# Kernel tuning notes

Measured on AMD Instinct MI355X. Metric: run time of the kernel, lower is better.

The kernel has to match this reference:

```python
import jax, jax.numpy as jnp
import numpy as np

N_NODES = 50000
N_EDGES = 800000
IN_CH = 128
HID = 128
NUM_GRAPHS = 512
BN_EPS = 1e-5


def setup_inputs() -> dict:
    key = jax.random.key(0)
    ks = jax.random.split(key, 16)
    x = jax.random.normal(ks[0], (N_NODES, IN_CH), dtype=jnp.float32)
    edge_index = jax.random.randint(ks[1], (2, N_EDGES), 0, N_NODES, dtype=jnp.int64)
    batch = jnp.sort(jax.random.randint(ks[2], (N_NODES,), 0, NUM_GRAPHS, dtype=jnp.int64))

    def glorot(k, shape):
        fan_in = shape[1]
        return jax.random.normal(k, shape, dtype=jnp.float32) / jnp.sqrt(jnp.float32(fan_in))

    # SAGEConv1: lin_l (aggr path, with bias), lin_r (root path, no bias)
    W1l = glorot(ks[3], (HID, IN_CH)); b1 = jnp.zeros((HID,), jnp.float32)
    W1r = glorot(ks[4], (HID, IN_CH))
    # SAGEConv2
    W2l = glorot(ks[5], (HID, HID)); b2 = jnp.zeros((HID,), jnp.float32)
    W2r = glorot(ks[6], (HID, HID))
    # MLP tail
    lin1_w = glorot(ks[7], (HID, HID)); lin1_b = jnp.zeros((HID,), jnp.float32)
    lin2_w = glorot(ks[8], (2, HID)); lin2_b = jnp.zeros((2,), jnp.float32)
    # BatchNorm1d (eval mode, running stats)
    gamma = jnp.ones((HID,), jnp.float32)
    beta = jnp.zeros((HID,), jnp.float32)
    running_mean = jax.random.normal(ks[9], (HID,), dtype=jnp.float32) * 0.1
    running_var = jax.random.uniform(ks[10], (HID,), dtype=jnp.float32, minval=0.5, maxval=1.5)
    return {
        "x": x, "edge_index": edge_index, "batch": batch,
        "W1l": W1l, "b1": b1, "W1r": W1r,
        "W2l": W2l, "b2": b2, "W2r": W2r,
        "lin1_w": lin1_w, "lin1_b": lin1_b,
        "lin2_w": lin2_w, "lin2_b": lin2_b,
        "gamma": gamma, "beta": beta,
        "running_mean": running_mean, "running_var": running_var,
    }


def _sage_conv(x, src, dst, Wl, bl, Wr):
    # mean-aggregate neighbor features (message flows src -> dst)
    n = x.shape[0]
    agg = jax.ops.segment_sum(x[src], dst, num_segments=n)  # [N, d]
    cnt = jax.ops.segment_sum(jnp.ones((src.shape[0], 1), x.dtype), dst, num_segments=n)
    mean = agg / jnp.maximum(cnt, 1.0)
    return mean @ Wl.T + bl + x @ Wr.T


def reference(x, edge_index, batch, W1l, b1, W1r, W2l, b2, W2r,
              lin1_w, lin1_b, lin2_w, lin2_b, gamma, beta,
              running_mean, running_var):
    src, dst = edge_index[0], edge_index[1]
    h = _sage_conv(x, src, dst, W1l, b1, W1r)      # [N, HID]
    h = _sage_conv(h, src, dst, W2l, b2, W2r)      # [N, HID]
    h = jax.ops.segment_sum(h, batch, num_segments=NUM_GRAPHS)  # global_add_pool -> [G, HID]
    h = h @ lin1_w.T + lin1_b
    # BatchNorm1d in eval mode (running stats)
    h = (h - running_mean) * jax.lax.rsqrt(running_var + BN_EPS) * gamma + beta
    h = jax.nn.relu(h)
    h = h @ lin2_w.T + lin2_b                      # [G, 2]
    # Dropout is identity in eval mode
    return h
```

## Files before the change

### kernel.cpp

```cpp
#include <hip/hip_runtime.h>
#include <hip/hip_bf16.h>

#define NN 50000
#define NE 800000
#define HID 128
#define NG 512
#define BN_EPS 1e-5f

typedef __attribute__((ext_vector_type(8))) short bf16x8;
typedef __attribute__((ext_vector_type(4))) float f32x4;

__device__ __forceinline__ ushort f2bf(float f) {
    uint u = __float_as_uint(f);
    uint r = (u + 0x7fffu + ((u >> 16) & 1u)) >> 16;
    return (ushort)r;
}
__device__ __forceinline__ float bf_lo(uint v) { return __uint_as_float(v << 16); }
__device__ __forceinline__ float bf_hi(uint v) { return __uint_as_float(v & 0xffff0000u); }

__global__ __launch_bounds__(256) void hist_kernel(const int* __restrict__ ei,
                                                   int E, int* __restrict__ deg,
                                                   int* __restrict__ rank) {
    int e = blockIdx.x * 256 + threadIdx.x;
    if (e >= E) return;
    int dst = ei[E + e];
    rank[e] = atomicAdd(&deg[dst], 1);
}

__global__ __launch_bounds__(256) void scan1_kernel(const int* __restrict__ deg,
                                                    int* __restrict__ row_start,
                                                    int* __restrict__ bsums, int n) {
    __shared__ int s[256];
    int i = blockIdx.x * 256 + threadIdx.x;
    int v = (i < n) ? deg[i] : 0;
    s[threadIdx.x] = v;
    __syncthreads();
    for (int off = 1; off < 256; off <<= 1) {
        int t = (threadIdx.x >= off) ? s[threadIdx.x - off] : 0;
        __syncthreads();
        s[threadIdx.x] += t;
        __syncthreads();
    }
    if (i < n) row_start[i] = s[threadIdx.x] - v;
    if (threadIdx.x == 255) bsums[blockIdx.x] = s[255];
}

__global__ __launch_bounds__(256) void scan2_kernel(int* __restrict__ bsums, int nb) {
    __shared__ int s[256];
    int v = (threadIdx.x < nb) ? bsums[threadIdx.x] : 0;
    s[threadIdx.x] = v;
    __syncthreads();
    for (int off = 1; off < 256; off <<= 1) {
        int t = (threadIdx.x >= off) ? s[threadIdx.x - off] : 0;
        __syncthreads();
        s[threadIdx.x] += t;
        __syncthreads();
    }
    if (threadIdx.x < nb) bsums[threadIdx.x] = s[threadIdx.x] - v;
}

__global__ __launch_bounds__(256) void scan3_kernel(int* __restrict__ row_start,
                                                    const int* __restrict__ bsums, int n) {
    int i = blockIdx.x * 256 + threadIdx.x;
    if (i < n) row_start[i] += bsums[blockIdx.x];
}

__global__ __launch_bounds__(256) void fill_kernel(const int* __restrict__ ei, int E,
                                                   const int* __restrict__ row_start,
                                                   const int* __restrict__ rank,
                                                   int* __restrict__ srclist) {
    int e = blockIdx.x * 256 + threadIdx.x;
    if (e >= E) return;
    int src = ei[e];
    int dst = ei[E + e];
    srclist[row_start[dst] + rank[e]] = src;
}

__global__ __launch_bounds__(256) void convert_bf16_kernel(const float* __restrict__ in,
                                                           ushort* __restrict__ out, int n4) {
    int i = blockIdx.x * 256 + threadIdx.x;
    if (i >= n4) return;
    float4 v = ((const float4*)in)[i];
    ushort4 o;
    o.x = f2bf(v.x);
    o.y = f2bf(v.y);
    o.z = f2bf(v.z);
    o.w = f2bf(v.w);
    ((ushort4*)out)[i] = o;
}

__global__ __launch_bounds__(64) void wprep_kernel(const float* __restrict__ W0,
                                                   const float* __restrict__ W1,
                                                   const float* __restrict__ W2,
                                                   const float* __restrict__ W3,
                                                   ushort* __restrict__ Wp) {
    int b = blockIdx.x;
    int m = b >> 5;
    int g = b & 31;
    int tile = g >> 2;
    int chunk = g & 3;
    int lane = threadIdx.x;
    const float* W = (m == 0) ? W0 : (m == 1) ? W1 : (m == 2) ? W2 : W3;
    int col = tile * 16 + (lane & 15);
    int k0 = chunk * 32 + (lane >> 4) * 8;
    ushort* dst = Wp + ((size_t)b * 64 + lane) * 8;
#pragma unroll
    for (int j = 0; j < 8; ++j) dst[j] = f2bf(W[col * HID + k0 + j]);
}

__global__ __launch_bounds__(256) void aggregate_kernel(const ushort* __restrict__ feat,
                                                        const int* __restrict__ row_start,
                                                        const int* __restrict__ deg,
                                                        const int* __restrict__ srclist,
                                                        ushort* __restrict__ mean, int n) {
    int node = blockIdx.x * 4 + (threadIdx.x >> 6);
    if (node >= n) return;
    int lane = threadIdx.x & 63;
    int cl = lane & 15;
    int sub = lane >> 4;
    const uint4* fb = (const uint4*)feat;
    int s0 = row_start[node];
    int d = deg[node];

    float a[8];
#pragma unroll
    for (int i = 0; i < 8; ++i) a[i] = 0.f;

    int j = 0;
    for (; j + 8 <= d; j += 8) {
        int i0 = srclist[s0 + j + sub];
        int i1 = srclist[s0 + j + 4 + sub];
        uint4 v0 = fb[(size_t)i0 * 16 + cl];
        uint4 v1 = fb[(size_t)i1 * 16 + cl];
        a[0] += bf_lo(v0.x) + bf_lo(v1.x);
        a[1] += bf_hi(v0.x) + bf_hi(v1.x);
        a[2] += bf_lo(v0.y) + bf_lo(v1.y);
        a[3] += bf_hi(v0.y) + bf_hi(v1.y);
        a[4] += bf_lo(v0.z) + bf_lo(v1.z);
        a[5] += bf_hi(v0.z) + bf_hi(v1.z);
        a[6] += bf_lo(v0.w) + bf_lo(v1.w);
        a[7] += bf_hi(v0.w) + bf_hi(v1.w);
    }
    for (; j < d; j += 4) {
        int idx = j + sub;
        bool valid = idx < d;
        int safe = valid ? idx : (d - 1);
        int src = srclist[s0 + safe];
        uint4 v = fb[(size_t)src * 16 + cl];
        float s = valid ? 1.f : 0.f;
        a[0] += s * bf_lo(v.x);
        a[1] += s * bf_hi(v.x);
        a[2] += s * bf_lo(v.y);
        a[3] += s * bf_hi(v.y);
        a[4] += s * bf_lo(v.z);
        a[5] += s * bf_hi(v.z);
        a[6] += s * bf_lo(v.w);
        a[7] += s * bf_hi(v.w);
    }

#pragma unroll
    for (int i = 0; i < 8; ++i) {
        float v = a[i];
        v += __shfl_xor(v, 16);
        v += __shfl_xor(v, 32);
        a[i] = v;
    }

    if (sub == 0) {
        float inv = 1.0f / fmaxf((float)d, 1.0f);
        uint4 o;
        o.x = (uint)f2bf(a[0] * inv) | ((uint)f2bf(a[1] * inv) << 16);
        o.y = (uint)f2bf(a[2] * inv) | ((uint)f2bf(a[3] * inv) << 16);
        o.z = (uint)f2bf(a[4] * inv) | ((uint)f2bf(a[5] * inv) << 16);
        o.w = (uint)f2bf(a[6] * inv) | ((uint)f2bf(a[7] * inv) << 16);
        ((uint4*)mean)[(size_t)node * 16 + cl] = o;
    }
}

template <bool POOL>
__global__ __launch_bounds__(256) void sage_gemm_mfma(const ushort* __restrict__ Amean,
                                                      const ushort* __restrict__ Aroot,
                                                      const ushort* __restrict__ WpL,
                                                      const float* __restrict__ bias,
                                                      const int* __restrict__ batch,
                                                      void* __restrict__ outv, int nwaves) {
    int w = blockIdx.x * 4 + (threadIdx.x >> 6);
    if (w >= nwaves) return;
    int lane = threadIdx.x & 63;
    int mrow = lane & 15;
    int quad = lane >> 4;
    int r0 = w * 16;

    f32x4 acc[8];
#pragma unroll
    for (int t = 0; t < 8; ++t) acc[t] = (f32x4){0.f, 0.f, 0.f, 0.f};

    const ushort* arow_m = Amean + ((size_t)(r0 + mrow)) * HID + quad * 8;
    const ushort* arow_r = Aroot + ((size_t)(r0 + mrow)) * HID + quad * 8;

#pragma unroll
    for (int half = 0; half < 2; ++half) {
        const ushort* arow = half ? arow_r : arow_m;
        const ushort* wb = WpL + (size_t)half * 16384 + (size_t)lane * 8;
#pragma unroll
        for (int c = 0; c < 4; ++c) {
            bf16x8 a = *(const bf16x8*)(arow + c * 32);
#pragma unroll
            for (int t = 0; t < 8; ++t) {
                bf16x8 b = *(const bf16x8*)(wb + (size_t)(t * 4 + c) * 512);
                acc[t] = __builtin_amdgcn_mfma_f32_16x16x32_bf16(a, b, acc[t], 0, 0, 0);
            }
        }
    }

    if (POOL) {
        float* pooled = (float*)outv;
        int rbase = r0 + quad * 4;
        int g0 = batch[rbase + 0];
        int g1 = batch[rbase + 1];
        int g2 = batch[rbase + 2];
        int g3 = batch[rbase + 3];
#pragma unroll
        for (int t = 0; t < 8; ++t) {
            int col = t * 16 + mrow;
            float bv = bias[col];
            float v0 = acc[t][0] + bv;
            float v1 = acc[t][1] + bv;
            float v2 = acc[t][2] + bv;
            float v3 = acc[t][3] + bv;
            int cg = g0;
            float s = v0;
            if (g1 == cg) s += v1; else { atomicAdd(&pooled[(size_t)cg * HID + col], s); cg = g1; s = v1; }
            if (g2 == cg) s += v2; else { atomicAdd(&pooled[(size_t)cg * HID + col], s); cg = g2; s = v2; }
            if (g3 == cg) s += v3; else { atomicAdd(&pooled[(size_t)cg * HID + col], s); cg = g3; s = v3; }
            atomicAdd(&pooled[(size_t)cg * HID + col], s);
        }
    } else {
        ushort* out = (ushort*)outv;
#pragma unroll
        for (int t = 0; t < 8; ++t) {
            int col = t * 16 + mrow;
            float bv = bias[col];
#pragma unroll
            for (int r = 0; r < 4; ++r) {
                int row = r0 + quad * 4 + r;
                out[(size_t)row * HID + col] = f2bf(acc[t][r] + bv);
            }
        }
    }
}

__global__ __launch_bounds__(128) void tail_kernel(const float* __restrict__ pooled,
                                                   const float* __restrict__ lin1_w,
                                                   const float* __restrict__ lin1_b,
                                                   const float* __restrict__ lin2_w,
                                                   const float* __restrict__ lin2_b,
                                                   const float* __restrict__ gamma,
                                                   const float* __restrict__ beta,
                                                   const float* __restrict__ rmean,
                                                   const float* __restrict__ rvar,
                                                   float* __restrict__ out) {
    __shared__ float Wt[64 * 128];
    __shared__ float p[128];
    __shared__ float tbuf[128];
    int g = blockIdx.x;
    int c = threadIdx.x;
    p[c] = pooled[g * HID + c];
    float acc = lin1_b[c];
    int kk = c & 63;
    int chalf = c >> 6;
    for (int k0 = 0; k0 < 128; k0 += 64) {
        __syncthreads();
        for (int i = 0; i < 64; ++i) {
            int crow = i * 2 + chalf;
            float v = lin1_w[crow * HID + k0 + kk];
            Wt[kk * 128 + (crow ^ (kk & 31))] = v;
        }
        __syncthreads();
#pragma unroll
        for (int k = 0; k < 64; ++k) {
            acc += p[k0 + k] * Wt[k * 128 + (c ^ (k & 31))];
        }
    }
    float v = (acc - rmean[c]) * rsqrtf(rvar[c] + BN_EPS) * gamma[c] + beta[c];
    v = fmaxf(v, 0.f);
    tbuf[c] = v;
    __syncthreads();
    int j = c >> 6;
    int lane = c & 63;
    float partial = tbuf[lane] * lin2_w[j * HID + lane] +
                    tbuf[lane + 64] * lin2_w[j * HID + lane + 64];
    for (int off = 32; off > 0; off >>= 1) partial += __shfl_down(partial, off);
    if (lane == 0) out[g * 2 + j] = partial + lin2_b[j];
}

extern "C" void kernel_launch(void* const* d_in, const int* in_sizes, int n_in,
                              void* d_out, int out_size, void* d_ws, size_t ws_size,
                              hipStream_t stream) {
    const float* x = (const float*)d_in[0];
    const int* ei = (const int*)d_in[1];
    const int* batch = (const int*)d_in[2];
    const float* W1l = (const float*)d_in[3];
    const float* b1 = (const float*)d_in[4];
    const float* W1r = (const float*)d_in[5];
    const float* W2l = (const float*)d_in[6];
    const float* b2 = (const float*)d_in[7];
    const float* W2r = (const float*)d_in[8];
    const float* lin1_w = (const float*)d_in[9];
    const float* lin1_b = (const float*)d_in[10];
    const float* lin2_w = (const float*)d_in[11];
    const float* lin2_b = (const float*)d_in[12];
    const float* gamma = (const float*)d_in[13];
    const float* beta = (const float*)d_in[14];
    const float* rmean = (const float*)d_in[15];
    const float* rvar = (const float*)d_in[16];
    float* out = (float*)d_out;

    const int N = NN, E = NE;
    const int NWAVES = N / 16;

    char* p = (char*)d_ws;
    auto carve = [&](size_t bytes) {
        void* r = (void*)p;
        p += (bytes + 255) & ~(size_t)255;
        return r;
    };
    int* deg = (int*)carve((size_t)N * 4);
    int* row_start = (int*)carve((size_t)N * 4);
    int* bsums = (int*)carve(1024 * 4);
    int* rank = (int*)carve((size_t)E * 4);
    int* srclist = (int*)carve((size_t)E * 4);
    ushort* xb = (ushort*)carve((size_t)N * HID * 2);
    ushort* meanb = (ushort*)carve((size_t)N * HID * 2);
    ushort* h1 = (ushort*)carve((size_t)N * HID * 2);
    float* pooled = (float*)carve((size_t)NG * HID * 4);
    ushort* Wp = (ushort*)carve(4 * 32 * 64 * 8 * 2);

    hipMemsetAsync(deg, 0, (size_t)N * 4, stream);
    hipMemsetAsync(pooled, 0, (size_t)NG * HID * 4, stream);

    const int scanBlocks = (N + 255) / 256;
    hist_kernel<<<(E + 255) / 256, 256, 0, stream>>>(ei, E, deg, rank);
    scan1_kernel<<<scanBlocks, 256, 0, stream>>>(deg, row_start, bsums, N);
    scan2_kernel<<<1, 256, 0, stream>>>(bsums, scanBlocks);
    scan3_kernel<<<scanBlocks, 256, 0, stream>>>(row_start, bsums, N);
    fill_kernel<<<(E + 255) / 256, 256, 0, stream>>>(ei, E, row_start, rank, srclist);

    convert_bf16_kernel<<<(N * HID / 4 + 255) / 256, 256, 0, stream>>>(x, xb, N * HID / 4);
    wprep_kernel<<<128, 64, 0, stream>>>(W1l, W1r, W2l, W2r, Wp);

    aggregate_kernel<<<(N + 3) / 4, 256, 0, stream>>>(xb, row_start, deg, srclist, meanb, N);
    sage_gemm_mfma<false><<<(NWAVES + 3) / 4, 256, 0, stream>>>(meanb, xb, Wp, b1, nullptr, h1,
                                                                NWAVES);
    aggregate_kernel<<<(N + 3) / 4, 256, 0, stream>>>(h1, row_start, deg, srclist, meanb, N);
    sage_gemm_mfma<true><<<(NWAVES + 3) / 4, 256, 0, stream>>>(meanb, h1, Wp + 32768, b2, batch,
                                                               pooled, NWAVES);
    tail_kernel<<<NG, 128, 0, stream>>>(pooled, lin1_w, lin1_b, lin2_w, lin2_b,
                                        gamma, beta, rmean, rvar, out);
}
```

Baseline: 271.3 us.

## Merge scan stages, fuse input/weight prep kernels, unroll aggregation gather by four

Folds scan2 and scan3 into one kernel where each block reduces the preceding block sums itself with wavefront shuffles, dropping a single-block launch. It also merges the x-to-bf16 conversion and weight packing into one launch, and widens the aggregation main loop to four neighbor gathers per iteration for more memory-level parallelism. The cost is redundant block-sum reductions in every scan block, and for low-degree nodes more edges fall through to the masked tail loop.

```diff
diff --git a/kernel.cpp b/kernel.cpp
--- a/kernel.cpp
+++ b/kernel.cpp
@@ -45,24 +45,17 @@
     if (threadIdx.x == 255) bsums[blockIdx.x] = s[255];
 }
 
-__global__ __launch_bounds__(256) void scan2_kernel(int* __restrict__ bsums, int nb) {
-    __shared__ int s[256];
-    int v = (threadIdx.x < nb) ? bsums[threadIdx.x] : 0;
-    s[threadIdx.x] = v;
+__global__ __launch_bounds__(256) void scan23_kernel(int* __restrict__ row_start,
+                                                     const int* __restrict__ bsums, int n) {
+    __shared__ int sred[4];
+    int v = (threadIdx.x < blockIdx.x) ? bsums[threadIdx.x] : 0;
+#pragma unroll
+    for (int off = 32; off > 0; off >>= 1) v += __shfl_xor(v, off);
+    if ((threadIdx.x & 63) == 0) sred[threadIdx.x >> 6] = v;
     __syncthreads();
-    for (int off = 1; off < 256; off <<= 1) {
-        int t = (threadIdx.x >= off) ? s[threadIdx.x - off] : 0;
-        __syncthreads();
-        s[threadIdx.x] += t;
-        __syncthreads();
-    }
-    if (threadIdx.x < nb) bsums[threadIdx.x] = s[threadIdx.x] - v;
-}
-
-__global__ __launch_bounds__(256) void scan3_kernel(int* __restrict__ row_start,
-                                                    const int* __restrict__ bsums, int n) {
+    int total = sred[0] + sred[1] + sred[2] + sred[3];
     int i = blockIdx.x * 256 + threadIdx.x;
-    if (i < n) row_start[i] += bsums[blockIdx.x];
+    if (i < n) row_start[i] += total;
 }
 
 __global__ __launch_bounds__(256) void fill_kernel(const int* __restrict__ ei, int E,
@@ -76,36 +69,38 @@
     srclist[row_start[dst] + rank[e]] = src;
 }
 
-__global__ __launch_bounds__(256) void convert_bf16_kernel(const float* __restrict__ in,
-                                                           ushort* __restrict__ out, int n4) {
-    int i = blockIdx.x * 256 + threadIdx.x;
-    if (i >= n4) return;
-    float4 v = ((const float4*)in)[i];
-    ushort4 o;
-    o.x = f2bf(v.x);
-    o.y = f2bf(v.y);
-    o.z = f2bf(v.z);
-    o.w = f2bf(v.w);
-    ((ushort4*)out)[i] = o;
-}
-
-__global__ __launch_bounds__(64) void wprep_kernel(const float* __restrict__ W0,
+#define CONV_BLOCKS 6250
+__global__ __launch_bounds__(256) void prep_kernel(const float* __restrict__ x,
+                                                   ushort* __restrict__ xb,
+                                                   const float* __restrict__ W0,
                                                    const float* __restrict__ W1,
                                                    const float* __restrict__ W2,
                                                    const float* __restrict__ W3,
                                                    ushort* __restrict__ Wp) {
-    int b = blockIdx.x;
-    int m = b >> 5;
-    int g = b & 31;
-    int tile = g >> 2;
-    int chunk = g & 3;
-    int lane = threadIdx.x;
-    const float* W = (m == 0) ? W0 : (m == 1) ? W1 : (m == 2) ? W2 : W3;
-    int col = tile * 16 + (lane & 15);
-    int k0 = chunk * 32 + (lane >> 4) * 8;
-    ushort* dst = Wp + ((size_t)b * 64 + lane) * 8;
-#pragma unroll
-    for (int j = 0; j < 8; ++j) dst[j] = f2bf(W[col * HID + k0 + j]);
+    if (blockIdx.x < CONV_BLOCKS) {
+        int i = blockIdx.x * 256 + threadIdx.x;
+        float4 v = ((const float4*)x)[i];
+        ushort4 o;
+        o.x = f2bf(v.x);
+        o.y = f2bf(v.y);
+        o.z = f2bf(v.z);
+        o.w = f2bf(v.w);
+        ((ushort4*)xb)[i] = o;
+    } else {
+        int b = (blockIdx.x - CONV_BLOCKS) * 4 + (threadIdx.x >> 6);
+        if (b >= 128) return;
+        int lane = threadIdx.x & 63;
+        int m = b >> 5;
+        int g = b & 31;
+        int tile = g >> 2;
+        int chunk = g & 3;
+        const float* W = (m == 0) ? W0 : (m == 1) ? W1 : (m == 2) ? W2 : W3;
+        int col = tile * 16 + (lane & 15);
+        int k0 = chunk * 32 + (lane >> 4) * 8;
+        ushort* dst = Wp + ((size_t)b * 64 + lane) * 8;
+#pragma unroll
+        for (int j = 0; j < 8; ++j) dst[j] = f2bf(W[col * HID + k0 + j]);
+    }
 }
 
 __global__ __launch_bounds__(256) void aggregate_kernel(const ushort* __restrict__ feat,
@@ -127,19 +122,23 @@
     for (int i = 0; i < 8; ++i) a[i] = 0.f;
 
     int j = 0;
-    for (; j + 8 <= d; j += 8) {
+    for (; j + 16 <= d; j += 16) {
         int i0 = srclist[s0 + j + sub];
         int i1 = srclist[s0 + j + 4 + sub];
+        int i2 = srclist[s0 + j + 8 + sub];
+        int i3 = srclist[s0 + j + 12 + sub];
         uint4 v0 = fb[(size_t)i0 * 16 + cl];
         uint4 v1 = fb[(size_t)i1 * 16 + cl];
-        a[0] += bf_lo(v0.x) + bf_lo(v1.x);
-        a[1] += bf_hi(v0.x) + bf_hi(v1.x);
-        a[2] += bf_lo(v0.y) + bf_lo(v1.y);
-        a[3] += bf_hi(v0.y) + bf_hi(v1.y);
-        a[4] += bf_lo(v0.z) + bf_lo(v1.z);
-        a[5] += bf_hi(v0.z) + bf_hi(v1.z);
-        a[6] += bf_lo(v0.w) + bf_lo(v1.w);
-        a[7] += bf_hi(v0.w) + bf_hi(v1.w);
+        uint4 v2 = fb[(size_t)i2 * 16 + cl];
+        uint4 v3 = fb[(size_t)i3 * 16 + cl];
+        a[0] += (bf_lo(v0.x) + bf_lo(v1.x)) + (bf_lo(v2.x) + bf_lo(v3.x));
+        a[1] += (bf_hi(v0.x) + bf_hi(v1.x)) + (bf_hi(v2.x) + bf_hi(v3.x));
+        a[2] += (bf_lo(v0.y) + bf_lo(v1.y)) + (bf_lo(v2.y) + bf_lo(v3.y));
+        a[3] += (bf_hi(v0.y) + bf_hi(v1.y)) + (bf_hi(v2.y) + bf_hi(v3.y));
+        a[4] += (bf_lo(v0.z) + bf_lo(v1.z)) + (bf_lo(v2.z) + bf_lo(v3.z));
+        a[5] += (bf_hi(v0.z) + bf_hi(v1.z)) + (bf_hi(v2.z) + bf_hi(v3.z));
+        a[6] += (bf_lo(v0.w) + bf_lo(v1.w)) + (bf_lo(v2.w) + bf_lo(v3.w));
+        a[7] += (bf_hi(v0.w) + bf_hi(v1.w)) + (bf_hi(v2.w) + bf_hi(v3.w));
     }
     for (; j < d; j += 4) {
         int idx = j + sub;
@@ -342,12 +341,10 @@
     const int scanBlocks = (N + 255) / 256;
     hist_kernel<<<(E + 255) / 256, 256, 0, stream>>>(ei, E, deg, rank);
     scan1_kernel<<<scanBlocks, 256, 0, stream>>>(deg, row_start, bsums, N);
-    scan2_kernel<<<1, 256, 0, stream>>>(bsums, scanBlocks);
-    scan3_kernel<<<scanBlocks, 256, 0, stream>>>(row_start, bsums, N);
+    scan23_kernel<<<scanBlocks, 256, 0, stream>>>(row_start, bsums, N);
     fill_kernel<<<(E + 255) / 256, 256, 0, stream>>>(ei, E, row_start, rank, srclist);
 
-    convert_bf16_kernel<<<(N * HID / 4 + 255) / 256, 256, 0, stream>>>(x, xb, N * HID / 4);
-    wprep_kernel<<<128, 64, 0, stream>>>(W1l, W1r, W2l, W2r, Wp);
+    prep_kernel<<<CONV_BLOCKS + 32, 256, 0, stream>>>(x, xb, W1l, W1r, W2l, W2r, Wp);
 
     aggregate_kernel<<<(N + 3) / 4, 256, 0, stream>>>(xb, row_start, deg, srclist, meanb, N);
     sage_gemm_mfma<false><<<(NWAVES + 3) / 4, 256, 0, stream>>>(meanb, xb, Wp, b1, nullptr, h1,
```

Result: no change. 271.1 us (-0.1%).
